# Kernel optimization log

Hardware: AMD Instinct MI355X
Metric: run time of the kernel (lower is better)

The kernel has to match this reference:

```python
import jax, jax.numpy as jnp
import numpy as np

MUL = 256  # multiplicity of each input-1 / output irrep
B = 131072  # batch (e.g. number of edges)

# Wigner-3j tensors for l <= 1 (e3nn convention: unit Frobenius norm)
_eye3 = np.eye(3, dtype=np.float32)
_eps = np.zeros((3, 3, 3), dtype=np.float32)
_eps[0, 1, 2] = _eps[1, 2, 0] = _eps[2, 0, 1] = 1.0
_eps[0, 2, 1] = _eps[2, 1, 0] = _eps[1, 0, 2] = -1.0
_S3 = np.float32(1.0 / np.sqrt(3.0))
W3J_000 = jnp.ones((1, 1, 1), jnp.float32)               # (i,j,k) for 0x0->0
W3J_110 = jnp.asarray(_eye3[:, :, None] * _S3)           # 1x1->0
W3J_011 = jnp.asarray(_eye3[None, :, :] * _S3)           # 0x1->1
W3J_101 = jnp.asarray(_eye3[:, None, :] * _S3)           # 1x0->1
W3J_111 = jnp.asarray(_eps / np.float32(np.sqrt(6.0)))   # 1x1->1

# path normalization: component norm (alpha=2l_out+1) / element path norm
C_OUT0 = float(np.sqrt(0.5))  # 2 paths feed 0e output: sqrt(1/2)
C_OUT1 = 1.0                  # 3 paths feed 1o output: sqrt(3/3)


def _path(w, w3j, x1, x2, pw):
    # w: (u,v)  w3j: (i,j,k)  x1: (z,u,i)  x2: (z,v,j)  ->  (z,u,k)
    return pw * jnp.einsum('uv,ijk,zui,zvj->zuk', w, w3j, x1, x2)


def setup_inputs() -> dict:
    key = jax.random.key(0)
    k1, k2, k3 = jax.random.split(key, 3)
    x = jax.random.normal(k1, (B, MUL * 4), dtype=jnp.float32)   # 256x0e + 256x1o
    y = jax.random.normal(k2, (B, 4), dtype=jnp.float32)        # 1x0e + 1x1o
    weight = jax.random.normal(k3, (5 * MUL,), dtype=jnp.float32)  # 5 uvu paths, path_shape (256,1)
    return {'x': x, 'y': y, 'weight': weight}


def reference(x, y, weight):
    z = x.shape[0]
    x0 = x[:, :MUL].reshape(z, MUL, 1)      # 256x0e
    x1 = x[:, MUL:].reshape(z, MUL, 3)      # 256x1o
    y0 = y[:, :1].reshape(z, 1, 1)          # 1x0e
    y1 = y[:, 1:].reshape(z, 1, 3)          # 1x1o
    ws = weight.reshape(5, MUL, 1)          # per-instruction (u,v) weights, in flat order
    # output irrep 0: 256x0e
    out0 = _path(ws[0], W3J_000, x0, y0, C_OUT0) + _path(ws[1], W3J_110, x1, y1, C_OUT0)
    # output irrep 1: 256x1o
    out1 = (_path(ws[2], W3J_011, x0, y1, C_OUT1)
            + _path(ws[3], W3J_101, x1, y0, C_OUT1)
            + _path(ws[4], W3J_111, x1, y1, C_OUT1))
    return jnp.concatenate([out0.reshape(z, MUL), out1.reshape(z, MUL * 3)], axis=1)
```

## Files before the change

kernel.cpp:

```cpp
#include <hip/hip_runtime.h>


namespace {

constexpr int MUL = 256;
constexpr int ROW = MUL * 4;

struct f3 { float x, y, z; };

__global__ __launch_bounds__(256) void tp_kernel(
    const float* __restrict__ x,
    const float* __restrict__ y,
    const float* __restrict__ w,
    float* __restrict__ out)
{
    const int z = blockIdx.x;
    const int u = threadIdx.x;

    const float4 yv = reinterpret_cast<const float4*>(y)[z];
    const float y0  = yv.x;
    const float y1x = yv.y, y1y = yv.z, y1z = yv.w;

    const float* xp = x   + (size_t)z * ROW;
    float*       op = out + (size_t)z * ROW;

    const float x0 = xp[u];
    const f3 x1 = reinterpret_cast<const f3*>(xp + MUL)[u];

    const float w0 = w[u];
    const float w1 = w[MUL + u];
    const float w2 = w[2 * MUL + u];
    const float w3 = w[3 * MUL + u];
    const float w4 = w[4 * MUL + u];

    constexpr float C0 = 0.70710678118654752f;
    constexpr float S3 = 0.57735026918962576f;
    constexpr float C6 = 0.40824829046386302f;

    const float dot = x1.x * y1x + x1.y * y1y + x1.z * y1z;
    const float cx  = x1.y * y1z - x1.z * y1y;
    const float cy  = x1.z * y1x - x1.x * y1z;
    const float cz  = x1.x * y1y - x1.y * y1x;

    op[u] = C0 * (w0 * x0 * y0 + S3 * w1 * dot);

    const float a = S3 * w2 * x0;
    const float b = S3 * w3 * y0;
    const float c = C6 * w4;
    f3 o1;
    o1.x = a * y1x + b * x1.x + c * cx;
    o1.y = a * y1y + b * x1.y + c * cy;
    o1.z = a * y1z + b * x1.z + c * cz;
    reinterpret_cast<f3*>(op + MUL)[u] = o1;
}

}

extern "C" void kernel_launch(void* const* d_in, const int* in_sizes, int n_in,
                              void* d_out, int out_size, void* d_ws, size_t ws_size,
                              hipStream_t stream) {
    const float* x = (const float*)d_in[0];
    const float* y = (const float*)d_in[1];
    const float* w = (const float*)d_in[2];
    float* out = (float*)d_out;

    const int B = in_sizes[0] / ROW;
    tp_kernel<<<B, MUL, 0, stream>>>(x, y, w, out);
}
```

Before: 813.0 us.

## Vectorize row I/O to float4 per lane with persistent grid-stride rows

Each 64-lane wavefront now handles one row, and each lane processes four multiplicity channels. It loads and stores them as 16-byte vectors, replacing scalar and 12-byte strided accesses. The kernel runs as a persistent grid of 2048 blocks that stride over rows. Weights are loaded once per thread instead of once per row, and non-temporal loads and stores are used for the streaming data. This targets memory-transaction efficiency and per-block overhead in a bandwidth-bound kernel, at the cost of more registers per thread.

```diff
diff --git a/kernel.cpp b/kernel.cpp
--- a/kernel.cpp
+++ b/kernel.cpp
@@ -3,55 +3,88 @@
 
 namespace {
 
-constexpr int MUL = 256;
-constexpr int ROW = MUL * 4;
+constexpr int MUL  = 256;
+constexpr int ROWF = MUL * 4;
+constexpr int ROW4 = MUL;
 
-struct f3 { float x, y, z; };
+constexpr float C0 = 0.70710678118654752f;
+constexpr float S3 = 0.57735026918962576f;
+constexpr float C6 = 0.40824829046386302f;
 
-__global__ __launch_bounds__(256) void tp_kernel(
-    const float* __restrict__ x,
-    const float* __restrict__ y,
-    const float* __restrict__ w,
-    float* __restrict__ out)
+using f4 = __attribute__((ext_vector_type(4))) float;
+
+struct TPOut { float o0, ox, oy, oz; };
+
+__device__ __forceinline__ TPOut tp1(
+    float x0, float x1x, float x1y, float x1z,
+    float y0, float y1x, float y1y, float y1z,
+    float w0, float w1, float w2, float w3, float w4)
 {
-    const int z = blockIdx.x;
-    const int u = threadIdx.x;
-
-    const float4 yv = reinterpret_cast<const float4*>(y)[z];
-    const float y0  = yv.x;
-    const float y1x = yv.y, y1y = yv.z, y1z = yv.w;
-
-    const float* xp = x   + (size_t)z * ROW;
-    float*       op = out + (size_t)z * ROW;
-
-    const float x0 = xp[u];
-    const f3 x1 = reinterpret_cast<const f3*>(xp + MUL)[u];
-
-    const float w0 = w[u];
-    const float w1 = w[MUL + u];
-    const float w2 = w[2 * MUL + u];
-    const float w3 = w[3 * MUL + u];
-    const float w4 = w[4 * MUL + u];
-
-    constexpr float C0 = 0.70710678118654752f;
-    constexpr float S3 = 0.57735026918962576f;
-    constexpr float C6 = 0.40824829046386302f;
-
-    const float dot = x1.x * y1x + x1.y * y1y + x1.z * y1z;
-    const float cx  = x1.y * y1z - x1.z * y1y;
-    const float cy  = x1.z * y1x - x1.x * y1z;
-    const float cz  = x1.x * y1y - x1.y * y1x;
-
-    op[u] = C0 * (w0 * x0 * y0 + S3 * w1 * dot);
-
+    const float dot = x1x * y1x + x1y * y1y + x1z * y1z;
+    const float cx  = x1y * y1z - x1z * y1y;
+    const float cy  = x1z * y1x - x1x * y1z;
+    const float cz  = x1x * y1y - x1y * y1x;
+    TPOut r;
+    r.o0 = C0 * (w0 * x0 * y0 + S3 * w1 * dot);
     const float a = S3 * w2 * x0;
     const float b = S3 * w3 * y0;
     const float c = C6 * w4;
-    f3 o1;
-    o1.x = a * y1x + b * x1.x + c * cx;
-    o1.y = a * y1y + b * x1.y + c * cy;
-    o1.z = a * y1z + b * x1.z + c * cz;
-    reinterpret_cast<f3*>(op + MUL)[u] = o1;
+    r.ox = a * y1x + b * x1x + c * cx;
+    r.oy = a * y1y + b * x1y + c * cy;
+    r.oz = a * y1z + b * x1z + c * cz;
+    return r;
+}
+
+__global__ __launch_bounds__(256) void tp_kernel(
+    const f4* __restrict__ x4,
+    const f4* __restrict__ y4,
+    const f4* __restrict__ wq,
+    f4* __restrict__ out4,
+    int nrows)
+{
+    const int lane = threadIdx.x & 63;
+    const int rsub = threadIdx.x >> 6;
+
+    const f4 w0  = wq[       lane];
+    const f4 w1  = wq[ 64 +  lane];
+    const f4 w2  = wq[128 +  lane];
+    const f4 w3  = wq[192 +  lane];
+    const f4 w4v = wq[256 +  lane];
+
+    const int zstride = gridDim.x * 4;
+    for (int z = blockIdx.x * 4 + rsub; z < nrows; z += zstride) {
+        const f4 yv = y4[z];
+        const float y0  = yv.x;
+        const float y1x = yv.y, y1y = yv.z, y1z = yv.w;
+
+        const f4* xr   = x4   + (size_t)z * ROW4;
+        f4*       orow = out4 + (size_t)z * ROW4;
+
+        const f4 x0q = __builtin_nontemporal_load(xr + lane);
+        const f4 xa  = __builtin_nontemporal_load(xr + 64 + 3 * lane);
+        const f4 xb  = __builtin_nontemporal_load(xr + 64 + 3 * lane + 1);
+        const f4 xc  = __builtin_nontemporal_load(xr + 64 + 3 * lane + 2);
+
+        const TPOut r0 = tp1(x0q.x, xa.x, xa.y, xa.z, y0, y1x, y1y, y1z,
+                             w0.x, w1.x, w2.x, w3.x, w4v.x);
+        const TPOut r1 = tp1(x0q.y, xa.w, xb.x, xb.y, y0, y1x, y1y, y1z,
+                             w0.y, w1.y, w2.y, w3.y, w4v.y);
+        const TPOut r2 = tp1(x0q.z, xb.z, xb.w, xc.x, y0, y1x, y1y, y1z,
+                             w0.z, w1.z, w2.z, w3.z, w4v.z);
+        const TPOut r3 = tp1(x0q.w, xc.y, xc.z, xc.w, y0, y1x, y1y, y1z,
+                             w0.w, w1.w, w2.w, w3.w, w4v.w);
+
+        f4 o0q, oa, ob, oc;
+        o0q.x = r0.o0; o0q.y = r1.o0; o0q.z = r2.o0; o0q.w = r3.o0;
+        oa.x = r0.ox;  oa.y = r0.oy;  oa.z = r0.oz;  oa.w = r1.ox;
+        ob.x = r1.oy;  ob.y = r1.oz;  ob.z = r2.ox;  ob.w = r2.oy;
+        oc.x = r2.oz;  oc.y = r3.ox;  oc.z = r3.oy;  oc.w = r3.oz;
+
+        __builtin_nontemporal_store(o0q, orow + lane);
+        __builtin_nontemporal_store(oa,  orow + 64 + 3 * lane);
+        __builtin_nontemporal_store(ob,  orow + 64 + 3 * lane + 1);
+        __builtin_nontemporal_store(oc,  orow + 64 + 3 * lane + 2);
+    }
 }
 
 }
@@ -59,11 +92,14 @@
 extern "C" void kernel_launch(void* const* d_in, const int* in_sizes, int n_in,
                               void* d_out, int out_size, void* d_ws, size_t ws_size,
                               hipStream_t stream) {
-    const float* x = (const float*)d_in[0];
-    const float* y = (const float*)d_in[1];
-    const float* w = (const float*)d_in[2];
-    float* out = (float*)d_out;
+    const f4* x = (const f4*)d_in[0];
+    const f4* y = (const f4*)d_in[1];
+    const f4* w = (const f4*)d_in[2];
+    f4* out = (f4*)d_out;
 
-    const int B = in_sizes[0] / ROW;
-    tp_kernel<<<B, MUL, 0, stream>>>(x, y, w, out);
+    const int B = in_sizes[0] / ROWF;
+
+    int blocks = 2048;
+    if (blocks * 4 > B) blocks = (B + 3) / 4;
+    tp_kernel<<<blocks, 256, 0, stream>>>(x, y, w, out, B);
 }
```

New measurement: 904.4 us. 1.11x slower.
